# Performance work log

Hardware: AMD Instinct MI355X
Metric: run time of the kernel (lower is better)

Reference implementation:

```python
import jax, jax.numpy as jnp
import numpy as np

B, T, D, F = 4, 1024, 256, 128  # input_dim=D, feature_dim=F, cat_size=1+F


def prelu(x, a):
    # torch.nn.PReLU with a single shared parameter (default init 0.25)
    return jnp.where(x >= 0, x, a * x)


def setup_inputs() -> dict:
    key = jax.random.key(0)
    ks = jax.random.split(key, 10)
    cat = 1 + F
    s1 = 1.0 / np.sqrt(cat)
    s2 = 1.0 / np.sqrt(F)
    return {
        "input": jax.random.normal(ks[0], (B, T, D), jnp.float32),
        "feature": jax.random.normal(ks[1], (B, T, F), jnp.float32),
        "slider": jax.random.uniform(ks[2], (B, T, 1), jnp.float32),
        "W1": jax.random.uniform(ks[3], (F, cat), jnp.float32, -s1, s1),
        "b1": jax.random.uniform(ks[4], (F,), jnp.float32, -s1, s1),
        "a1": jnp.float32(0.25),
        "W2": jax.random.uniform(ks[5], (F, F), jnp.float32, -s2, s2),
        "b2": jax.random.uniform(ks[6], (F,), jnp.float32, -s2, s2),
        "a2": jnp.float32(0.25),
        "Wp": jax.random.uniform(ks[7], (2, cat), jnp.float32, -s1, s1),
        "bp": jax.random.uniform(ks[8], (2,), jnp.float32, -s1, s1),
    }


def reference(input, feature, slider, W1, b1, a1, W2, b2, a2, Wp, bp):
    # input: (B,T,D) -> (B,T,D,1); feature broadcast over D: (B,T,1,F)
    inp = input[..., None]                       # (B,T,D,1)
    feat = feature[..., None, :]                 # (B,T,1,F)
    feat = jnp.broadcast_to(feat, (B, T, D, F))  # repeat across input_dim
    x = jnp.concatenate((inp, feat), axis=-1)    # (B,T,D,1+F)
    # tmlp: Linear -> PReLU -> Linear -> PReLU
    h = prelu(jnp.einsum('btdc,fc->btdf', x, W1) + b1, a1)  # (B,T,D,F)
    h = prelu(jnp.einsum('btdf,gf->btdg', h, W2) + b2, a2)  # (B,T,D,F)
    y = jnp.concatenate((h, inp), axis=-1)       # (B,T,D,1+F)
    p = jnp.einsum('btdc,oc->btdo', y, Wp) + bp  # (B,T,D,2)
    g = p[..., 0:1] * jax.nn.sigmoid(p[..., 1:2])  # GLU(dim=-1) -> (B,T,D,1)
    return (inp * (1.0 + g)).squeeze(-1)         # (B,T,D)
```

## Files before the change

### kernel.cpp

```cpp
#include <hip/hip_runtime.h>
#include <hip/hip_bf16.h>

#define BT 4096
#define DD 256
#define CAT 129

typedef __attribute__((ext_vector_type(8))) _Float16 f16x8;
typedef __attribute__((ext_vector_type(4))) _Float16 f16x4;
typedef __attribute__((ext_vector_type(2))) _Float16 h2;
typedef __attribute__((ext_vector_type(4))) float f32x4;

static __device__ __forceinline__ h2 cvt_pk(float a, float b) {
    return __builtin_bit_cast(h2, __builtin_amdgcn_cvt_pkrtz(a, b));
}

static __device__ __forceinline__ float fdot2f(h2 a, h2 b, float c) {
#if __has_builtin(__builtin_amdgcn_fdot2)
    return __builtin_amdgcn_fdot2(__builtin_bit_cast(__fp16 __attribute__((ext_vector_type(2))), a),
                                  __builtin_bit_cast(__fp16 __attribute__((ext_vector_type(2))), b),
                                  c, false);
#else
    return fmaf((float)a[0], (float)b[0], fmaf((float)a[1], (float)b[1], c));
#endif
}

__global__ void __launch_bounds__(256) k_cvt(
    const float* __restrict__ W1, const float* __restrict__ W2,
    _Float16* __restrict__ w2h, _Float16* __restrict__ w1h,
    _Float16* __restrict__ w10h)
{
    const int t = threadIdx.x, b = blockIdx.x;
    if (b < 8) {
        #pragma unroll
        for (int i = 0; i < 8; ++i) {
            int idx = b * 2048 + i * 256 + t;
            w2h[idx] = (_Float16)W2[idx];
        }
    } else {
        int q = b - 8;
        #pragma unroll
        for (int i = 0; i < 8; ++i) {
            int idx = q * 2048 + i * 256 + t;
            int f = idx >> 7, c = idx & 127;
            w1h[idx ^ ((f & 7) << 3)] = (_Float16)W1[f * CAT + 1 + c];
        }
        if (q == 0 && t < 128) w10h[t] = (_Float16)W1[t * CAT];
    }
}

__global__ void __launch_bounds__(256) k_prep2(
    const float* __restrict__ feature, const _Float16* __restrict__ w1h,
    const float* __restrict__ b1p, _Float16* __restrict__ v1h)
{
    __shared__ __align__(16) _Float16 fS[2048];
    const int t = threadIdx.x;
    const int r0 = blockIdx.x * 16;

    {
        int e = t * 8;
        int r = e >> 7, c = e & 127;
        const float4* src = (const float4*)(feature + (size_t)(r0 + r) * 128 + c);
        float4 x0 = src[0], x1 = src[1];
        f16x8 hv;
        hv[0] = (_Float16)x0.x; hv[1] = (_Float16)x0.y;
        hv[2] = (_Float16)x0.z; hv[3] = (_Float16)x0.w;
        hv[4] = (_Float16)x1.x; hv[5] = (_Float16)x1.y;
        hv[6] = (_Float16)x1.z; hv[7] = (_Float16)x1.w;
        *(f16x8*)&fS[e ^ ((r & 7) << 3)] = hv;
    }
    __syncthreads();

    const int lane = t & 63, wv = t >> 6;
    const int l15 = lane & 15, l4 = lane >> 4;

    f16x8 bfr[2][4];
    float4 b1v[2];
    #pragma unroll
    for (int nt = 0; nt < 2; ++nt) {
        const int f0 = wv * 32 + nt * 16;
        b1v[nt] = *(const float4*)(b1p + f0 + l4 * 4);
        #pragma unroll
        for (int kc = 0; kc < 4; ++kc) {
            int f = f0 + l15, c = kc * 32 + l4 * 8;
            bfr[nt][kc] = *(const f16x8*)&w1h[(f * 128 + c) ^ ((f & 7) << 3)];
        }
    }

    const f32x4 fz = {0.f, 0.f, 0.f, 0.f};
    f32x4 acc[2] = {fz, fz};
    #pragma unroll
    for (int kc = 0; kc < 4; ++kc) {
        int r = l15, c = kc * 32 + l4 * 8;
        f16x8 afr = *(const f16x8*)&fS[(r * 128 + c) ^ ((r & 7) << 3)];
        #pragma unroll
        for (int nt = 0; nt < 2; ++nt)
            acc[nt] = __builtin_amdgcn_mfma_f32_16x16x32_f16(
                bfr[nt][kc], afr, acc[nt], 0, 0, 0);
    }

    #pragma unroll
    for (int nt = 0; nt < 2; ++nt) {
        f16x4 o;
        o[0] = (_Float16)(acc[nt][0] + ((const float*)&b1v[nt])[0]);
        o[1] = (_Float16)(acc[nt][1] + ((const float*)&b1v[nt])[1]);
        o[2] = (_Float16)(acc[nt][2] + ((const float*)&b1v[nt])[2]);
        o[3] = (_Float16)(acc[nt][3] + ((const float*)&b1v[nt])[3]);
        *(f16x4*)&v1h[(size_t)(r0 + l15) * 128 + wv * 32 + nt * 16 + l4 * 4] = o;
    }
}

__global__ void __launch_bounds__(512, 4) k_main(
    const float* __restrict__ inp, const float* __restrict__ b2p,
    const float* __restrict__ Wp, const float* __restrict__ bpp,
    const float* __restrict__ a1p, const float* __restrict__ a2p,
    const _Float16* __restrict__ v1h, const _Float16* __restrict__ w2h,
    const _Float16* __restrict__ w10h, float* __restrict__ out)
{
    __shared__ float inps[512];
    __shared__ float2 prs[2][4][64];

    const int tid  = threadIdx.x;
    const int lane = tid & 63, wv = tid >> 6;
    const int rg   = wv >> 2, cg = wv & 3;
    const int l15  = lane & 15, l4 = lane >> 4;
    const int bt0  = blockIdx.x * 2;

    inps[tid] = inp[(size_t)bt0 * DD + tid];

    f16x8 bfr[2][4];
    #pragma unroll
    for (int nt = 0; nt < 2; ++nt)
        #pragma unroll
        for (int kc = 0; kc < 4; ++kc)
            bfr[nt][kc] = *(const f16x8*)
                &w2h[(cg * 32 + nt * 16 + l15) * 128 + kc * 32 + l4 * 8];

    f16x8 w10pk[4];
    #pragma unroll
    for (int kc = 0; kc < 4; ++kc)
        w10pk[kc] = *(const f16x8*)&w10h[kc * 32 + l4 * 8];

    const _Float16 a1s = (_Float16)a1p[0];
    const _Float16 a2s = (_Float16)a2p[0];
    f16x8 a1x8 = {a1s, a1s, a1s, a1s, a1s, a1s, a1s, a1s};
    h2 a2v; a2v[0] = a2s; a2v[1] = a2s;
    const float wpi0 = Wp[128], wpi1 = Wp[CAT + 128];
    const float bp0  = bpp[0],  bp1  = bpp[1];

    f32x4 accInit[2];
    h2 wpa_pk[2][2], wpb_pk[2][2];
    #pragma unroll
    for (int nt = 0; nt < 2; ++nt) {
        const int g0 = cg * 32 + nt * 16 + l4 * 4;
        accInit[nt][0] = b2p[g0];     accInit[nt][1] = b2p[g0 + 1];
        accInit[nt][2] = b2p[g0 + 2]; accInit[nt][3] = b2p[g0 + 3];
        wpa_pk[nt][0] = cvt_pk(Wp[g0],           Wp[g0 + 1]);
        wpa_pk[nt][1] = cvt_pk(Wp[g0 + 2],       Wp[g0 + 3]);
        wpb_pk[nt][0] = cvt_pk(Wp[CAT + g0],     Wp[CAT + g0 + 1]);
        wpb_pk[nt][1] = cvt_pk(Wp[CAT + g0 + 2], Wp[CAT + g0 + 3]);
    }
    __syncthreads();

    f16x8 v1pk[4];

    #pragma unroll 2
    for (int i = 0; i < 8; ++i) {
        const int btl = i >> 2, qt = i & 3, buf = i & 1;

        if ((i & 3) == 0) {
            #pragma unroll
            for (int kc = 0; kc < 4; ++kc)
                v1pk[kc] = *(const f16x8*)
                    &v1h[(size_t)(bt0 + btl) * 128 + kc * 32 + l4 * 8];
        }

        const int rbase = btl * 256 + qt * 64 + rg * 32;
        const float s0f = inps[rbase + l15];
        const float s1f = inps[rbase + 16 + l15];
        const _Float16 sh0 = (_Float16)s0f, sh1 = (_Float16)s1f;
        f16x8 s8a = {sh0, sh0, sh0, sh0, sh0, sh0, sh0, sh0};
        f16x8 s8b = {sh1, sh1, sh1, sh1, sh1, sh1, sh1, sh1};

        f32x4 acc[2][2];
        acc[0][0] = accInit[0]; acc[0][1] = accInit[0];
        acc[1][0] = accInit[1]; acc[1][1] = accInit[1];

        #pragma unroll
        for (int kc = 0; kc < 4; ++kc) {
            f16x8 h0 = v1pk[kc] + w10pk[kc] * s8a;
            f16x8 af0 = __builtin_elementwise_max(h0, a1x8 * h0);
            f16x8 h1 = v1pk[kc] + w10pk[kc] * s8b;
            f16x8 af1 = __builtin_elementwise_max(h1, a1x8 * h1);
            #pragma unroll
            for (int nt = 0; nt < 2; ++nt) {
                acc[nt][0] = __builtin_amdgcn_mfma_f32_16x16x32_f16(
                    bfr[nt][kc], af0, acc[nt][0], 0, 0, 0);
                acc[nt][1] = __builtin_amdgcn_mfma_f32_16x16x32_f16(
                    bfr[nt][kc], af1, acc[nt][1], 0, 0, 0);
            }
        }

        #pragma unroll
        for (int rt = 0; rt < 2; ++rt) {
            float p0 = 0.f, p1 = 0.f;
            #pragma unroll
            for (int nt = 0; nt < 2; ++nt) {
                h2 hh0 = cvt_pk(acc[nt][rt][0], acc[nt][rt][1]);
                h2 hh1 = cvt_pk(acc[nt][rt][2], acc[nt][rt][3]);
                h2 hp0 = __builtin_elementwise_max(hh0, a2v * hh0);
                h2 hp1 = __builtin_elementwise_max(hh1, a2v * hh1);
                p0 = fdot2f(wpa_pk[nt][0], hp0, p0);
                p0 = fdot2f(wpa_pk[nt][1], hp1, p0);
                p1 = fdot2f(wpb_pk[nt][0], hp0, p1);
                p1 = fdot2f(wpb_pk[nt][1], hp1, p1);
            }
            p0 += __shfl_xor(p0, 16); p0 += __shfl_xor(p0, 32);
            p1 += __shfl_xor(p1, 16); p1 += __shfl_xor(p1, 32);
            if (l4 == 0) {
                float2 v; v.x = p0; v.y = p1;
                prs[buf][cg][rg * 32 + rt * 16 + l15] = v;
            }
        }
        __syncthreads();

        if (wv == i) {
            const float s = inps[btl * 256 + qt * 64 + lane];
            const float2 t0 = prs[buf][0][lane], t1 = prs[buf][1][lane];
            const float2 t2 = prs[buf][2][lane], t3 = prs[buf][3][lane];
            const float e0 = t0.x + t1.x + t2.x + t3.x + wpi0 * s + bp0;
            const float e1 = t0.y + t1.y + t2.y + t3.y + wpi1 * s + bp1;
            const float gg = e0 / (1.f + __expf(-e1));
            out[(size_t)(bt0 + btl) * DD + qt * 64 + lane] = s * (1.f + gg);
        }
    }
}

extern "C" void kernel_launch(void* const* d_in, const int* in_sizes, int n_in,
                              void* d_out, int out_size, void* d_ws, size_t ws_size,
                              hipStream_t stream)
{
    (void)in_sizes; (void)n_in; (void)out_size; (void)ws_size;
    const float* input   = (const float*)d_in[0];
    const float* feature = (const float*)d_in[1];
    const float* W1 = (const float*)d_in[3];
    const float* b1 = (const float*)d_in[4];
    const float* a1 = (const float*)d_in[5];
    const float* W2 = (const float*)d_in[6];
    const float* b2 = (const float*)d_in[7];
    const float* a2 = (const float*)d_in[8];
    const float* Wp = (const float*)d_in[9];
    const float* bp = (const float*)d_in[10];
    float* out = (float*)d_out;

    _Float16* v1h  = (_Float16*)d_ws;
    _Float16* w2h  = v1h + (size_t)BT * 128;
    _Float16* w1h  = w2h + 16384;
    _Float16* w10h = w1h + 16384;

    k_cvt  <<<dim3(16),   dim3(256), 0, stream>>>(W1, W2, w2h, w1h, w10h);
    k_prep2<<<dim3(256),  dim3(256), 0, stream>>>(feature, w1h, b1, v1h);
    k_main <<<dim3(2048), dim3(512), 0, stream>>>(input, b2, Wp, bp, a1, a2,
                                                  v1h, w2h, w10h, out);
}
```

Before: 71.60 us.

## Split main kernel into sync-free per-wave partial GEMM and separate finalize pass

Each wave now owns one (b,t) row and half the output features (64 columns), looping over all 256 d positions with 4 N-tiles, writing packed fp16 partial projections to a workspace. The GLU/output combine moves to a new k_fin kernel that sums the two halves. This removes the shared-memory staging and per-iteration __syncthreads of the old 512-thread block, at the cost of an extra launch, a global round trip of partials, and fp16 rounding of the partial sums. The b2 bias is now added in fp16 after the MFMA instead of seeding the accumulator.

```diff
diff --git a/kernel.cpp b/kernel.cpp
--- a/kernel.cpp
+++ b/kernel.cpp
@@ -109,130 +109,114 @@
     }
 }
 
-__global__ void __launch_bounds__(512, 4) k_main(
+__global__ void __launch_bounds__(256, 3) k_main(
     const float* __restrict__ inp, const float* __restrict__ b2p,
-    const float* __restrict__ Wp, const float* __restrict__ bpp,
-    const float* __restrict__ a1p, const float* __restrict__ a2p,
-    const _Float16* __restrict__ v1h, const _Float16* __restrict__ w2h,
-    const _Float16* __restrict__ w10h, float* __restrict__ out)
-{
-    __shared__ float inps[512];
-    __shared__ float2 prs[2][4][64];
-
+    const float* __restrict__ Wp, const float* __restrict__ a1p,
+    const float* __restrict__ a2p, const _Float16* __restrict__ v1h,
+    const _Float16* __restrict__ w2h, const _Float16* __restrict__ w10h,
+    unsigned* __restrict__ pr)
+{
     const int tid  = threadIdx.x;
     const int lane = tid & 63, wv = tid >> 6;
-    const int rg   = wv >> 2, cg = wv & 3;
     const int l15  = lane & 15, l4 = lane >> 4;
-    const int bt0  = blockIdx.x * 2;
-
-    inps[tid] = inp[(size_t)bt0 * DD + tid];
-
-    f16x8 bfr[2][4];
-    #pragma unroll
-    for (int nt = 0; nt < 2; ++nt)
+    const int W    = blockIdx.x * 4 + wv;
+    const int cg   = W & 1, bt = W >> 1;
+
+    f16x8 bfr[4][4];
+    #pragma unroll
+    for (int nt = 0; nt < 4; ++nt)
         #pragma unroll
         for (int kc = 0; kc < 4; ++kc)
             bfr[nt][kc] = *(const f16x8*)
-                &w2h[(cg * 32 + nt * 16 + l15) * 128 + kc * 32 + l4 * 8];
-
-    f16x8 w10pk[4];
-    #pragma unroll
-    for (int kc = 0; kc < 4; ++kc)
+                &w2h[(cg * 64 + nt * 16 + l15) * 128 + kc * 32 + l4 * 8];
+
+    f16x8 v1pk[4], w10pk[4];
+    #pragma unroll
+    for (int kc = 0; kc < 4; ++kc) {
+        v1pk[kc]  = *(const f16x8*)&v1h[(size_t)bt * 128 + kc * 32 + l4 * 8];
         w10pk[kc] = *(const f16x8*)&w10h[kc * 32 + l4 * 8];
+    }
+
+    h2 b2pk[4][2], wpapk[4][2], wpbpk[4][2];
+    #pragma unroll
+    for (int nt = 0; nt < 4; ++nt) {
+        const int g0 = cg * 64 + nt * 16 + l4 * 4;
+        const float4 bv = *(const float4*)&b2p[g0];
+        const float4 wa = *(const float4*)&Wp[g0];
+        b2pk[nt][0]  = cvt_pk(bv.x, bv.y);  b2pk[nt][1]  = cvt_pk(bv.z, bv.w);
+        wpapk[nt][0] = cvt_pk(wa.x, wa.y);  wpapk[nt][1] = cvt_pk(wa.z, wa.w);
+        wpbpk[nt][0] = cvt_pk(Wp[CAT + g0],     Wp[CAT + g0 + 1]);
+        wpbpk[nt][1] = cvt_pk(Wp[CAT + g0 + 2], Wp[CAT + g0 + 3]);
+    }
 
     const _Float16 a1s = (_Float16)a1p[0];
     const _Float16 a2s = (_Float16)a2p[0];
-    f16x8 a1x8 = {a1s, a1s, a1s, a1s, a1s, a1s, a1s, a1s};
+    const f16x8 a1x8 = {a1s, a1s, a1s, a1s, a1s, a1s, a1s, a1s};
     h2 a2v; a2v[0] = a2s; a2v[1] = a2s;
+    const f32x4 fz = {0.f, 0.f, 0.f, 0.f};
+
+    const float* srow = inp + (size_t)bt * DD;
+    float s_cur = srow[l15];
+
+    #pragma unroll 2
+    for (int it = 0; it < 16; ++it) {
+        const float s_row = s_cur;
+        if (it < 15) s_cur = srow[(it + 1) * 16 + l15];
+
+        const _Float16 sh = (_Float16)s_row;
+        const f16x8 s8 = {sh, sh, sh, sh, sh, sh, sh, sh};
+
+        f32x4 acc[4] = {fz, fz, fz, fz};
+        #pragma unroll
+        for (int kc = 0; kc < 4; ++kc) {
+            f16x8 h  = v1pk[kc] + w10pk[kc] * s8;
+            f16x8 af = __builtin_elementwise_max(h, a1x8 * h);
+            #pragma unroll
+            for (int nt = 0; nt < 4; ++nt)
+                acc[nt] = __builtin_amdgcn_mfma_f32_16x16x32_f16(
+                    bfr[nt][kc], af, acc[nt], 0, 0, 0);
+        }
+
+        float p0 = 0.f, p1 = 0.f;
+        #pragma unroll
+        for (int nt = 0; nt < 4; ++nt) {
+            h2 hh0 = cvt_pk(acc[nt][0], acc[nt][1]) + b2pk[nt][0];
+            h2 hh1 = cvt_pk(acc[nt][2], acc[nt][3]) + b2pk[nt][1];
+            h2 hp0 = __builtin_elementwise_max(hh0, a2v * hh0);
+            h2 hp1 = __builtin_elementwise_max(hh1, a2v * hh1);
+            p0 = fdot2f(wpapk[nt][0], hp0, p0);
+            p0 = fdot2f(wpapk[nt][1], hp1, p0);
+            p1 = fdot2f(wpbpk[nt][0], hp0, p1);
+            p1 = fdot2f(wpbpk[nt][1], hp1, p1);
+        }
+
+        p0 += __shfl_xor(p0, 16); p0 += __shfl_xor(p0, 32);
+        p1 += __shfl_xor(p1, 16); p1 += __shfl_xor(p1, 32);
+
+        if (l4 == 0)
+            pr[((size_t)bt * DD + it * 16 + l15) * 2 + cg] =
+                __builtin_bit_cast(unsigned, cvt_pk(p0, p1));
+    }
+}
+
+__global__ void __launch_bounds__(256) k_fin(
+    const float* __restrict__ inp, const float* __restrict__ Wp,
+    const float* __restrict__ bpp, const unsigned* __restrict__ pr,
+    float* __restrict__ out)
+{
+    const int i = blockIdx.x * 256 + threadIdx.x;
     const float wpi0 = Wp[128], wpi1 = Wp[CAT + 128];
     const float bp0  = bpp[0],  bp1  = bpp[1];
 
-    f32x4 accInit[2];
-    h2 wpa_pk[2][2], wpb_pk[2][2];
-    #pragma unroll
-    for (int nt = 0; nt < 2; ++nt) {
-        const int g0 = cg * 32 + nt * 16 + l4 * 4;
-        accInit[nt][0] = b2p[g0];     accInit[nt][1] = b2p[g0 + 1];
-        accInit[nt][2] = b2p[g0 + 2]; accInit[nt][3] = b2p[g0 + 3];
-        wpa_pk[nt][0] = cvt_pk(Wp[g0],           Wp[g0 + 1]);
-        wpa_pk[nt][1] = cvt_pk(Wp[g0 + 2],       Wp[g0 + 3]);
-        wpb_pk[nt][0] = cvt_pk(Wp[CAT + g0],     Wp[CAT + g0 + 1]);
-        wpb_pk[nt][1] = cvt_pk(Wp[CAT + g0 + 2], Wp[CAT + g0 + 3]);
-    }
-    __syncthreads();
-
-    f16x8 v1pk[4];
-
-    #pragma unroll 2
-    for (int i = 0; i < 8; ++i) {
-        const int btl = i >> 2, qt = i & 3, buf = i & 1;
-
-        if ((i & 3) == 0) {
-            #pragma unroll
-            for (int kc = 0; kc < 4; ++kc)
-                v1pk[kc] = *(const f16x8*)
-                    &v1h[(size_t)(bt0 + btl) * 128 + kc * 32 + l4 * 8];
-        }
-
-        const int rbase = btl * 256 + qt * 64 + rg * 32;
-        const float s0f = inps[rbase + l15];
-        const float s1f = inps[rbase + 16 + l15];
-        const _Float16 sh0 = (_Float16)s0f, sh1 = (_Float16)s1f;
-        f16x8 s8a = {sh0, sh0, sh0, sh0, sh0, sh0, sh0, sh0};
-        f16x8 s8b = {sh1, sh1, sh1, sh1, sh1, sh1, sh1, sh1};
-
-        f32x4 acc[2][2];
-        acc[0][0] = accInit[0]; acc[0][1] = accInit[0];
-        acc[1][0] = accInit[1]; acc[1][1] = accInit[1];
-
-        #pragma unroll
-        for (int kc = 0; kc < 4; ++kc) {
-            f16x8 h0 = v1pk[kc] + w10pk[kc] * s8a;
-            f16x8 af0 = __builtin_elementwise_max(h0, a1x8 * h0);
-            f16x8 h1 = v1pk[kc] + w10pk[kc] * s8b;
-            f16x8 af1 = __builtin_elementwise_max(h1, a1x8 * h1);
-            #pragma unroll
-            for (int nt = 0; nt < 2; ++nt) {
-                acc[nt][0] = __builtin_amdgcn_mfma_f32_16x16x32_f16(
-                    bfr[nt][kc], af0, acc[nt][0], 0, 0, 0);
-                acc[nt][1] = __builtin_amdgcn_mfma_f32_16x16x32_f16(
-                    bfr[nt][kc], af1, acc[nt][1], 0, 0, 0);
-            }
-        }
-
-        #pragma unroll
-        for (int rt = 0; rt < 2; ++rt) {
-            float p0 = 0.f, p1 = 0.f;
-            #pragma unroll
-            for (int nt = 0; nt < 2; ++nt) {
-                h2 hh0 = cvt_pk(acc[nt][rt][0], acc[nt][rt][1]);
-                h2 hh1 = cvt_pk(acc[nt][rt][2], acc[nt][rt][3]);
-                h2 hp0 = __builtin_elementwise_max(hh0, a2v * hh0);
-                h2 hp1 = __builtin_elementwise_max(hh1, a2v * hh1);
-                p0 = fdot2f(wpa_pk[nt][0], hp0, p0);
-                p0 = fdot2f(wpa_pk[nt][1], hp1, p0);
-                p1 = fdot2f(wpb_pk[nt][0], hp0, p1);
-                p1 = fdot2f(wpb_pk[nt][1], hp1, p1);
-            }
-            p0 += __shfl_xor(p0, 16); p0 += __shfl_xor(p0, 32);
-            p1 += __shfl_xor(p1, 16); p1 += __shfl_xor(p1, 32);
-            if (l4 == 0) {
-                float2 v; v.x = p0; v.y = p1;
-                prs[buf][cg][rg * 32 + rt * 16 + l15] = v;
-            }
-        }
-        __syncthreads();
-
-        if (wv == i) {
-            const float s = inps[btl * 256 + qt * 64 + lane];
-            const float2 t0 = prs[buf][0][lane], t1 = prs[buf][1][lane];
-            const float2 t2 = prs[buf][2][lane], t3 = prs[buf][3][lane];
-            const float e0 = t0.x + t1.x + t2.x + t3.x + wpi0 * s + bp0;
-            const float e1 = t0.y + t1.y + t2.y + t3.y + wpi1 * s + bp1;
-            const float gg = e0 / (1.f + __expf(-e1));
-            out[(size_t)(bt0 + btl) * DD + qt * 64 + lane] = s * (1.f + gg);
-        }
-    }
+    const uint2 v = ((const uint2*)pr)[i];
+    const h2 pa = __builtin_bit_cast(h2, v.x);
+    const h2 pb = __builtin_bit_cast(h2, v.y);
+    const float s = inp[i];
+
+    const float e0 = (float)pa[0] + (float)pb[0] + wpi0 * s + bp0;
+    const float e1 = (float)pa[1] + (float)pb[1] + wpi1 * s + bp1;
+    const float gg = e0 / (1.f + __expf(-e1));
+    out[i] = s * (1.f + gg);
 }
 
 extern "C" void kernel_launch(void* const* d_in, const int* in_sizes, int n_in,
@@ -252,13 +236,15 @@
     const float* bp = (const float*)d_in[10];
     float* out = (float*)d_out;
 
-    _Float16* v1h  = (_Float16*)d_ws;
-    _Float16* w2h  = v1h + (size_t)BT * 128;
-    _Float16* w1h  = w2h + 16384;
-    _Float16* w10h = w1h + 16384;
+    unsigned*  pr   = (unsigned*)d_ws;
+    _Float16*  v1h  = (_Float16*)((char*)d_ws + (size_t)BT * DD * 8);
+    _Float16*  w2h  = v1h + (size_t)BT * 128;
+    _Float16*  w1h  = w2h + 16384;
+    _Float16*  w10h = w1h + 16384;
 
     k_cvt  <<<dim3(16),   dim3(256), 0, stream>>>(W1, W2, w2h, w1h, w10h);
     k_prep2<<<dim3(256),  dim3(256), 0, stream>>>(feature, w1h, b1, v1h);
-    k_main <<<dim3(2048), dim3(512), 0, stream>>>(input, b2, Wp, bp, a1, a2,
-                                                  v1h, w2h, w10h, out);
-}
+    k_main <<<dim3(2048), dim3(256), 0, stream>>>(input, b2, Wp, a1, a2,
+                                                  v1h, w2h, w10h, pr);
+    k_fin  <<<dim3(4096), dim3(256), 0, stream>>>(input, Wp, bp, pr, out);
+}
```

New measurement: 68.75 us. 1.04x faster.
